# Kernel tuning notes

Measured on AMD Instinct MI355X. Metric: run time of the kernel, lower is better.

The kernel has to match this reference:

```python
import jax
import jax.numpy as jnp
from jax import lax
import numpy as np


def _corr(xs, ks, pad):
    """All-pairs 2D cross-correlation, per sample.

    xs: [N, A, H, W]  (side that gets zero-padded / shifted)
    ks: [N, B, H, W]  (kernels)
    returns out[n, a, b, u, v] = sum_{h,w} xs[n, a, h+u-pad, w+v-pad] * ks[n, b, h, w]
    with u, v in [0, 2*pad].
    """
    xp = jnp.pad(xs, ((0, 0), (0, 0), (pad, pad), (pad, pad)))

    def one(xp1, k1):
        # xp1: [A, H+2p, W+2p] -> lhs batch=A; k1: [B, H, W] -> B output filters
        return lax.conv_general_dilated(
            xp1[:, None], k1[:, None], (1, 1), 'VALID',
            dimension_numbers=('NCHW', 'OIHW', 'NCHW'))  # [A, B, 2p+1-?, ...]

    return jax.vmap(one)(xp, ks)  # [N, A, B, out_h, out_w]


@jax.custom_vjp
def cholesky_solve(Q, P):
    L = jnp.linalg.cholesky(Q)
    return jax.scipy.linalg.cho_solve((L, True), P)


def _chol_fwd(Q, P):
    L = jnp.linalg.cholesky(Q)
    D = jax.scipy.linalg.cho_solve((L, True), P)
    return D, (L, D)


def _chol_bwd(res, g):
    L, D = res
    dP = jax.scipy.linalg.cho_solve((L, True), g)
    dQ = -jnp.matmul(dP, jnp.swapaxes(D, -1, -2))
    return (dQ, dP)


cholesky_solve.defvjp(_chol_fwd, _chol_bwd)


def setup_inputs() -> dict:
    key = jax.random.key(0)
    k1, k2, k3 = jax.random.split(key, 3)
    N, C_in, C_out, H, W, ds = 4, 64, 4, 96, 96, 5
    x = jax.random.normal(k1, (N, 1, C_in, H, W), dtype=jnp.float32)
    d = jax.random.normal(k2, (N, C_out, C_in, ds, ds), dtype=jnp.float32)
    y = jax.random.normal(k3, (N, C_out, 1, H, W), dtype=jnp.float32)
    alpha = jnp.ones((N, 1, 1, 1), dtype=jnp.float32)
    reg = jnp.ones((1,), dtype=jnp.float32)
    return {"x": x, "d": d, "y": y, "alpha": alpha, "reg": reg}


def reference(x, d, y, alpha, reg):
    # DSBlock.forward: solve per-sample regularized normal equations for the dictionary d.
    xs = x[:, 0]      # [N, C_in, H, W]
    ys = y[:, :, 0]   # [N, C_out, H, W]
    N, C_in, H, W = xs.shape
    C_out, ds = d.shape[1], d.shape[-1]
    K = C_in * ds * ds

    # xtx_raw[n, j, i, u, v] = sum_{h,w} x[n,i,h+u-(ds-1), w+v-(ds-1)] * x[n,j,h,w]
    corr = _corr(xs, xs, ds - 1).transpose(0, 2, 1, 3, 4)  # [N, j, i, 2ds-1, 2ds-1]

    # Q[n,(j,kh,kw),(i,ph,pw)] = corr[n,j,i, ph-kh+ds-1, pw-kw+ds-1]
    # (equivalent to the original unfold + flip + fancy-index permutation chain)
    idx = jnp.arange(ds)
    u = idx[None, :] - idx[:, None] + (ds - 1)  # u[k, p] = p - k + ds - 1
    Q6 = corr[:, :, :, u[:, None, :, None], u[None, :, None, :]]  # [N,j,i,kh,kw,ph,pw]
    Q = Q6.transpose(0, 1, 3, 4, 2, 5, 6).reshape(N, K, K)        # symmetric Gram

    # xty[n, i, co, u, v] = sum_{h,w} x[n,i,h+u-p, w+v-p] * y[n,co,h,w], p=(ds-1)//2
    xty = _corr(xs, ys, (ds - 1) // 2)            # [N, i, co, ds, ds]
    P = xty.transpose(0, 1, 3, 4, 2).reshape(N, K, C_out)

    # diagonal regularization: alpha * H * W * reg / (ds^2 * C_in)
    a = alpha.reshape(N) * H * W * reg[0] / (ds * ds * C_in)  # [N]
    Q = Q + a[:, None, None] * jnp.eye(K, dtype=Q.dtype)
    P = P + a[:, None, None] * d.transpose(0, 2, 3, 4, 1).reshape(N, K, C_out)

    D = cholesky_solve(Q, P)                      # [N, K, C_out]
    return D.reshape(N, C_in, ds, ds, C_out).transpose(0, 4, 1, 2, 3)
```

## Files before the change

kernel.cpp:

```cpp
#include <hip/hip_runtime.h>

#define NS   4
#define CIN  64
#define COUT 4
#define HH   96
#define WW   96
#define HWSZ 9216
#define DS   5
#define KD   1600
#define ITER 6

#define TROWB 192
#define TCHB  (96*TROWB)
#define TIMGB ((size_t)64*TCHB)
#define TSB   ((size_t)256*TCHB)
#define CORR_RS 84

#define SKC  12
#define RB   8

#define CSTR  104
#define SLOTB (64*CSTR)

#define XAOFF 0
#define XBOFF 79872
#define XBSLOT (32*CSTR)

typedef _Float16 f16_t;
typedef _Float16 f16x8_t __attribute__((ext_vector_type(8)));
typedef float    f32x16_t __attribute__((ext_vector_type(16)));

static __device__ __forceinline__ float4 f4add(float4 a, float4 b) {
  return make_float4(a.x + b.x, a.y + b.y, a.z + b.z, a.w + b.w);
}
static __device__ __forceinline__ float4 f4sub(float4 a, float4 b) {
  return make_float4(a.x - b.x, a.y - b.y, a.z - b.z, a.w - b.w);
}
static __device__ __forceinline__ float4 f4mul(float4 a, float4 b) {
  return make_float4(a.x * b.x, a.y * b.y, a.z * b.z, a.w * b.w);
}
static __device__ __forceinline__ float4 f4div(float4 a, float4 b) {
  return make_float4(a.x / b.x, a.y / b.y, a.z / b.z, a.w / b.w);
}
static __device__ __forceinline__ float4 f4fma(float4 a, float4 b, float4 c) {
  return make_float4(fmaf(a.x, b.x, c.x), fmaf(a.y, b.y, c.y),
                     fmaf(a.z, b.z, c.z), fmaf(a.w, b.w, c.w));
}
static __device__ __forceinline__ float f4sel(float4 v, int c) {
  return c == 0 ? v.x : c == 1 ? v.y : c == 2 ? v.z : v.w;
}
static __device__ __forceinline__ unsigned int packh2(float a, float b) {
  f16_t h0 = (f16_t)a, h1 = (f16_t)b;
  return (unsigned int)__builtin_bit_cast(unsigned short, h0)
       | ((unsigned int)__builtin_bit_cast(unsigned short, h1) << 16);
}

__global__ __launch_bounds__(256) void convert_kernel(const float* __restrict__ xs,
                                                      const float* __restrict__ ys,
                                                      unsigned int* __restrict__ TS32,
                                                      unsigned int* __restrict__ YS32) {
  const int PER = 256 * 96 * 48;
  const int TSTOT = 5 * PER;
  int idx = blockIdx.x * 256 + threadIdx.x;
  if (idx < TSTOT) {
    int s = idx / PER;
    int rr = idx - s * PER;
    int p = rr % 48; int t = rr / 48;
    int r = t % 96;  int cg = t / 96;
    const float* row = xs + (size_t)cg * HWSZ + r * 96;
    int j0 = 2 * p, j1 = j0 + 1;
    float f0 = (j0 + s < 96) ? row[j0 + s] : 0.f;
    float f1 = (j1 + s < 96) ? row[j1 + s] : 0.f;
    TS32[idx] = packh2(f0, f1);
  } else {
    int i2 = idx - TSTOT;
    if (i2 >= 5 * 16 * 96 * 48) return;
    int v  = i2 / 73728;
    int r3 = i2 % 73728;
    int nb = r3 / 4608;
    int r4 = r3 % 4608;
    int r = r4 / 48, p = r4 % 48;
    const float* row = ys + (size_t)nb * HWSZ + r * 96;
    int c0 = 2 * p + 2 - v, c1 = c0 + 1;
    float f0 = (c0 >= 0 && c0 < 96) ? row[c0] : 0.f;
    float f1 = (c1 >= 0 && c1 < 96) ? row[c1] : 0.f;
    YS32[i2] = packh2(f0, f1);
  }
}

__global__ __launch_bounds__(256, 1) void partial_kernel(const unsigned short* __restrict__ TS,
                                                         const unsigned short* __restrict__ YS,
                                                         float* __restrict__ corrPart,
                                                         float* __restrict__ xtyPart) {
  __shared__ __align__(16) unsigned char lds[24 * SLOTB];
  int bid = blockIdx.x;
  int tid = threadIdx.x, wid = tid >> 6, lane = tid & 63;
  int l5 = lane >> 5, l31 = lane & 31;

  if (bid < 240) {
    int n = bid & 3;
    int rest = bid >> 2;
    int sv = rest % 5;
    int kc = rest / 5;
    int r0 = kc * RB;
    int mt = wid >> 1, nt = wid & 1;
    const char* Abase = (const char*)TS + (size_t)n * TIMGB;
    const char* Bbase = (const char*)TS + (size_t)sv * TSB + (size_t)n * TIMGB;
    f32x16_t acc[9] = {};

    for (int kh = 0; kh < 2; ++kh) {
      if (kh) __syncthreads();
      for (int bb = 0; bb < 3; ++bb) {
        uint4 tmp[12];
#pragma unroll
        for (int i = 0; i < 12; ++i) {
          int q = (bb * 12 + i) * 256 + tid;
          int slot = q / 384;
          int rem = q - slot * 384;
          int ch = rem / 6, sub = rem - ch * 6;
          bool isA = slot < 16;
          int row = isA ? (r0 - 4 + slot) : (r0 + slot - 16);
          uint4 v = make_uint4(0u, 0u, 0u, 0u);
          if (row >= 0 && row < 96) {
            const char* src = (isA ? Abase : Bbase)
                            + (size_t)ch * TCHB + (size_t)row * TROWB + kh * 96 + sub * 16;
            v = *(const uint4*)src;
          }
          tmp[i] = v;
        }
#pragma unroll
        for (int i = 0; i < 12; ++i) {
          int q = (bb * 12 + i) * 256 + tid;
          int slot = q / 384;
          int rem = q - slot * 384;
          int ch = rem / 6, sub = rem - ch * 6;
          char* dst = (char*)lds + slot * SLOTB + ch * CSTR + sub * 16;
          *(uint2*)dst = make_uint2(tmp[i].x, tmp[i].y);
          *(uint2*)(dst + 8) = make_uint2(tmp[i].z, tmp[i].w);
        }
      }
      __syncthreads();

      int ca = mt * 32 + l31, cb = nt * 32 + l31;
#pragma unroll
      for (int ktl = 0; ktl < 3; ++ktl) {
        int ko = ktl * 32 + l5 * 16;
        auto frag = [&](int slot, int ch) -> f16x8_t {
          const char* p = (const char*)lds + slot * SLOTB + ch * CSTR + ko;
          uint2 lo = *(const uint2*)p;
          uint2 hi = *(const uint2*)(p + 8);
          uint4 u = make_uint4(lo.x, lo.y, hi.x, hi.y);
          return __builtin_bit_cast(f16x8_t, u);
        };
        f16x8_t ring[9];
#pragma unroll
        for (int t = 0; t < 9; ++t) ring[t] = frag(t, ca);
#pragma unroll
        for (int r = 0; r < 8; ++r) {
          f16x8_t b = frag(16 + r, cb);
#pragma unroll
          for (int du = 0; du < 9; ++du) {
            acc[du] = __builtin_amdgcn_mfma_f32_32x32x16_f16(
                ring[(r + 8 - du) % 9], b, acc[du], 0, 0, 0);
          }
          if (r < 7) ring[r % 9] = frag(r + 9, ca);
        }
      }
    }
#pragma unroll
    for (int du = 0; du < 9; ++du) {
      float* outp = corrPart + (((size_t)(sv * 9 + du) * SKC + kc) * 4 + n) * 4096;
#pragma unroll
      for (int rg = 0; rg < 16; ++rg) {
        int m  = mt * 32 + (rg & 3) + 8 * (rg >> 2) + 4 * l5;
        int nn = nt * 32 + l31;
        outp[m * 64 + nn] = acc[du][rg];
      }
    }
    return;
  }

  int id = bid - 240;
  int n = id & 3, kc = id >> 2;
  int r0 = kc * RB;
  int mt = wid & 1, rh = wid >> 1;
  const char* Ab = (const char*)TS + (size_t)n * TIMGB;
  const char* Yb = (const char*)YS;
  f32x16_t acc[5] = {};

  for (int kh = 0; kh < 2; ++kh) {
    if (kh) __syncthreads();
    for (int bb = 0; bb < 2; ++bb) {
      uint4 tmp[12];
#pragma unroll
      for (int i = 0; i < 12; ++i) {
        int q = (bb * 12 + i) * 256 + tid;
        uint4 val = make_uint4(0u, 0u, 0u, 0u);
        if (q < 4608) {
          int slot = q / 384, rem = q % 384, ch = rem / 6, sub = rem % 6;
          int grow = r0 - 2 + slot;
          if (grow >= 0 && grow < 96)
            val = *(const uint4*)(Ab + (size_t)ch * TCHB + (size_t)grow * TROWB + kh * 96 + sub * 16);
        } else if (q < 5568) {
          int qq = q - 4608;
          int j = qq / 120, rem = qq % 120, col = rem / 6, sub = rem % 6;
          int b = col / 5, v = col % 5;
          int grow = r0 + j;
          val = *(const uint4*)(Yb + ((size_t)(v * 16 + n * 4 + b) * 96 + grow) * 192 + kh * 96 + sub * 16);
        }
        tmp[i] = val;
      }
#pragma unroll
      for (int i = 0; i < 12; ++i) {
        int q = (bb * 12 + i) * 256 + tid;
        char* dst;
        if (q < 4608) {
          int slot = q / 384, rem = q % 384, ch = rem / 6, sub = rem % 6;
          dst = (char*)lds + XAOFF + slot * SLOTB + ch * CSTR + sub * 16;
        } else {
          int j, col, sub;
          if (q < 5568) { int qq = q - 4608; j = qq / 120; int rem = qq % 120; col = rem / 6; sub = rem % 6; }
          else          { int q2 = q - 5568; j = q2 / 72;  int rem = q2 % 72;  col = 20 + rem / 6; sub = rem % 6; }
          dst = (char*)lds + XBOFF + j * XBSLOT + col * CSTR + sub * 16;
        }
        *(uint2*)dst = make_uint2(tmp[i].x, tmp[i].y);
        *(uint2*)(dst + 8) = make_uint2(tmp[i].z, tmp[i].w);
      }
    }
    __syncthreads();

    int ca = mt * 32 + l31;
    int jb = rh * 4;
#pragma unroll
    for (int ktl = 0; ktl < 3; ++ktl) {
      int ko = ktl * 32 + l5 * 16;
      auto fragA = [&](int slot) -> f16x8_t {
        const char* p = (const char*)lds + XAOFF + slot * SLOTB + ca * CSTR + ko;
        uint2 lo = *(const uint2*)p; uint2 hi = *(const uint2*)(p + 8);
        return __builtin_bit_cast(f16x8_t, make_uint4(lo.x, lo.y, hi.x, hi.y));
      };
      auto fragB = [&](int j) -> f16x8_t {
        const char* p = (const char*)lds + XBOFF + j * XBSLOT + l31 * CSTR + ko;
        uint2 lo = *(const uint2*)p; uint2 hi = *(const uint2*)(p + 8);
        return __builtin_bit_cast(f16x8_t, make_uint4(lo.x, lo.y, hi.x, hi.y));
      };
#pragma unroll
      for (int jj = 0; jj < 4; ++jj) {
        f16x8_t b  = fragB(jb + jj);
        f16x8_t a0 = fragA(jb + jj + 0);
        f16x8_t a1 = fragA(jb + jj + 1);
        f16x8_t a2 = fragA(jb + jj + 2);
        f16x8_t a3 = fragA(jb + jj + 3);
        f16x8_t a4 = fragA(jb + jj + 4);
        acc[0] = __builtin_amdgcn_mfma_f32_32x32x16_f16(a0, b, acc[0], 0, 0, 0);
        acc[1] = __builtin_amdgcn_mfma_f32_32x32x16_f16(a1, b, acc[1], 0, 0, 0);
        acc[2] = __builtin_amdgcn_mfma_f32_32x32x16_f16(a2, b, acc[2], 0, 0, 0);
        acc[3] = __builtin_amdgcn_mfma_f32_32x32x16_f16(a3, b, acc[3], 0, 0, 0);
        acc[4] = __builtin_amdgcn_mfma_f32_32x32x16_f16(a4, b, acc[4], 0, 0, 0);
      }
    }
  }

  __syncthreads();
  float* scr = (float*)lds;
#pragma unroll
  for (int u = 0; u < 5; ++u)
#pragma unroll
    for (int rg = 0; rg < 16; ++rg) {
      int m = mt * 32 + (rg & 3) + 8 * (rg >> 2) + 4 * l5;
      scr[rh * 10240 + u * 2048 + m * 32 + l31] = acc[u][rg];
    }
  __syncthreads();
  float* outp = xtyPart + (size_t)(n * SKC + kc) * 5 * 2048;
  for (int e = tid; e < 10240; e += 256)
    outp[e] = scr[e] + scr[10240 + e];
}

__global__ __launch_bounds__(256) void reduce_kernel(const float* __restrict__ corrPart,
                                                     float* __restrict__ corrP,
                                                     const float* __restrict__ xtyPart,
                                                     const float* __restrict__ dd,
                                                     const float* __restrict__ alpha,
                                                     const float* __restrict__ reg,
                                                     float* __restrict__ P) {
  int bid0 = blockIdx.x;
  if (bid0 < 164) {
    int n = bid0 / 41, p = bid0 % 41;
    int du, dv;
    if (p < 36) { du = p % 9; dv = 5 + p / 9; }
    else        { du = p - 36; dv = 4; }
    int t = (p < 36) ? (9 + p) : (p - 36);
    int o1 = du * 9 + dv, o2 = (8 - du) * 9 + (8 - dv);
    bool mir = !(du == 4 && dv == 4);
    for (int e = threadIdx.x; e < 4096; e += 256) {
      float s = 0.f;
#pragma unroll
      for (int kc = 0; kc < SKC; ++kc)
        s += corrPart[(((size_t)t * SKC + kc) * 4 + n) * 4096 + e];
      int m = e >> 6, nn = e & 63;
      corrP[((size_t)(n * 64 + m) * 64 + nn) * CORR_RS + o1] = s;
      if (mir) corrP[((size_t)(n * 64 + nn) * 64 + m) * CORR_RS + o2] = s;
    }
    return;
  }
  int idx = (bid0 - 164) * 256 + threadIdx.x;
  int b = idx & 3;
  int row = (idx >> 2) % KD;
  int n = idx / 6400;
  int c = row / 25;
  int uv = row % 25;
  int u = uv / 5, v = uv % 5;
  float s = 0.f;
#pragma unroll
  for (int kc = 0; kc < SKC; ++kc)
    s += xtyPart[((size_t)(n * SKC + kc) * 5 + u) * 2048 + c * 32 + b * 5 + v];
  float a = alpha[n] * reg[0] * ((float)(HH * WW) / (float)(DS * DS * CIN));
  float dvv = dd[((size_t)(n * COUT + b) * CIN + c) * 25 + uv];
  P[idx] = s + a * dvv;
}

static __device__ __forceinline__ void allreduce2_f4(float4& a, float4& b,
                                                     float4* redA, float4* redB, int tid) {
#pragma unroll
  for (int off = 1; off < 64; off <<= 1) {
    a.x += __shfl_xor(a.x, off); a.y += __shfl_xor(a.y, off);
    a.z += __shfl_xor(a.z, off); a.w += __shfl_xor(a.w, off);
    b.x += __shfl_xor(b.x, off); b.y += __shfl_xor(b.y, off);
    b.z += __shfl_xor(b.z, off); b.w += __shfl_xor(b.w, off);
  }
  int wid = tid >> 6;
  if ((tid & 63) == 0) { redA[wid] = a; redB[wid] = b; }
  __syncthreads();
  float4 sa = f4add(f4add(redA[0], redA[1]), f4add(redA[2], redA[3]));
  float4 sb = f4add(f4add(redB[0], redB[1]), f4add(redB[2], redB[3]));
  __syncthreads();
  a = sa; b = sb;
}

static __device__ __forceinline__ void allreduce4_f4(float4& a, float4& b, float4& c, float4& d,
                                                     float4 (*red)[4], int tid) {
#pragma unroll
  for (int off = 1; off < 64; off <<= 1) {
    a.x += __shfl_xor(a.x, off); a.y += __shfl_xor(a.y, off);
    a.z += __shfl_xor(a.z, off); a.w += __shfl_xor(a.w, off);
    b.x += __shfl_xor(b.x, off); b.y += __shfl_xor(b.y, off);
    b.z += __shfl_xor(b.z, off); b.w += __shfl_xor(b.w, off);
    c.x += __shfl_xor(c.x, off); c.y += __shfl_xor(c.y, off);
    c.z += __shfl_xor(c.z, off); c.w += __shfl_xor(c.w, off);
    d.x += __shfl_xor(d.x, off); d.y += __shfl_xor(d.y, off);
    d.z += __shfl_xor(d.z, off); d.w += __shfl_xor(d.w, off);
  }
  int wid = tid >> 6;
  if ((tid & 63) == 0) { red[wid][0] = a; red[wid][1] = b; red[wid][2] = c; red[wid][3] = d; }
  __syncthreads();
  float4 sa = f4add(f4add(red[0][0], red[1][0]), f4add(red[2][0], red[3][0]));
  float4 sb = f4add(f4add(red[0][1], red[1][1]), f4add(red[2][1], red[3][1]));
  float4 sc = f4add(f4add(red[0][2], red[1][2]), f4add(red[2][2], red[3][2]));
  float4 sd = f4add(f4add(red[0][3], red[1][3]), f4add(red[2][3], red[3][3]));
  __syncthreads();
  a = sa; b = sb; c = sc; d = sd;
}

__global__ __launch_bounds__(256) void cg_iter_kernel(
    const float* __restrict__ corrP, const float* __restrict__ P,
    const float* __restrict__ Rin, float* __restrict__ Rout,
    const float* __restrict__ Win, float* __restrict__ Wout,
    const float* __restrict__ PFin, float* __restrict__ PFout,
    float* __restrict__ X,
    const float* __restrict__ ralpha, const float* __restrict__ rreg,
    int first) {
  __shared__ float4 pS[KD];
  __shared__ float4 red4[4][4];
  __shared__ float redW[4][25][4];

  int b = blockIdx.x;
  int n = b >> 6, c1 = b & 63;
  int tid = threadIdx.x;

  const float4* Rin4 = (const float4*)Rin + (size_t)n * KD;
  const float4* Win4 = (const float4*)Win + (size_t)n * KD;
  const float4* PFin4 = (const float4*)PFin + (size_t)n * KD;
  const float4* P4 = (const float4*)P + (size_t)n * KD;
  float4* Rout4 = (float4*)Rout + (size_t)n * KD;
  float4* PFout4 = (float4*)PFout + (size_t)n * KD;
  float4* X4 = (float4*)X + (size_t)n * KD;

  const float4 zero4 = make_float4(0.f, 0.f, 0.f, 0.f);
  float4 rv[7], wv[7], pv[7];
#pragma unroll
  for (int t = 0; t < 7; ++t) {
    int idx = tid + 256 * t;
    bool ok = idx < KD;
    if (first) {
      rv[t] = ok ? P4[idx] : zero4;
      wv[t] = zero4; pv[t] = zero4;
    } else {
      rv[t] = ok ? Rin4[idx] : zero4;
      wv[t] = ok ? Win4[idx] : zero4;
      pv[t] = ok ? PFin4[idx] : zero4;
    }
  }
  float4 rho = zero4, pAp = zero4, rw = zero4, ww = zero4;
#pragma unroll
  for (int t = 0; t < 7; ++t) {
    rho = f4fma(rv[t], rv[t], rho);
    pAp = f4fma(pv[t], wv[t], pAp);
    rw  = f4fma(rv[t], wv[t], rw);
    ww  = f4fma(wv[t], wv[t], ww);
  }
  allreduce4_f4(rho, pAp, rw, ww, red4, tid);

  float4 av = first ? zero4 : f4div(rho, pAp);
  float4 two_rw = f4add(rw, rw);
  float4 inner = f4sub(two_rw, f4mul(av, ww));
  float4 rho_k = f4sub(rho, f4mul(av, inner));
  float4 bv = first ? zero4 : f4div(rho_k, rho);

  int lo = c1 * 25;
#pragma unroll
  for (int t = 0; t < 7; ++t) {
    int idx = tid + 256 * t;
    if (idx < KD) {
      rv[t] = f4sub(rv[t], f4mul(av, wv[t]));
      float4 pnew = f4fma(bv, pv[t], rv[t]);
      if (idx >= lo && idx < lo + 25) {
        if (first) X4[idx] = zero4;
        else X4[idx] = f4fma(av, pv[t], X4[idx]);
        PFout4[idx] = pnew;
        Rout4[idx] = rv[t];
      }
      pS[idx] = pnew;
    }
  }
  __syncthreads();

  int c2 = tid >> 2, col = tid & 3;
  const float4* crow4 = (const float4*)(corrP + (((size_t)(n * 64 + c1)) * 64 + c2) * CORR_RS);
  float creg[81];
#pragma unroll
  for (int t4 = 0; t4 < 20; ++t4) *(float4*)&creg[4 * t4] = crow4[t4];
  creg[80] = ((const float*)crow4)[80];

  float a25[25];
#pragma unroll
  for (int i = 0; i < 25; ++i) a25[i] = 0.f;
  const float* pSf = (const float*)pS;
#pragma unroll
  for (int j = 0; j < 25; ++j) {
    float pvv = pSf[(c2 * 25 + j) * 4 + col];
#pragma unroll
    for (int i = 0; i < 25; ++i) {
      const int i1 = i / 5, i2 = i % 5, j1 = j / 5, j2 = j % 5;
      a25[i] += creg[(j1 - i1 + 4) * 9 + (j2 - i2 + 4)] * pvv;
    }
  }
#pragma unroll
  for (int i = 0; i < 25; ++i) {
    float v = a25[i];
    v += __shfl_xor(v, 4); v += __shfl_xor(v, 8);
    v += __shfl_xor(v, 16); v += __shfl_xor(v, 32);
    a25[i] = v;
  }
  int wid = tid >> 6;
  if ((tid & 63) < 4) {
#pragma unroll
    for (int i = 0; i < 25; ++i) redW[wid][i][col] = a25[i];
  }
  __syncthreads();
  if (tid < 100) {
    int i = tid >> 2, cc = tid & 3;
    float wval = redW[0][i][cc] + redW[1][i][cc] + redW[2][i][cc] + redW[3][i][cc];
    float aa = ralpha[n] * rreg[0] * ((float)(HH * WW) / (float)(DS * DS * CIN));
    int row = lo + i;
    wval = fmaf(aa, pSf[row * 4 + cc], wval);
    Wout[((size_t)n * KD + row) * 4 + cc] = wval;
  }
}

__global__ __launch_bounds__(256) void cg_final_kernel(
    const float* __restrict__ Rin, const float* __restrict__ Win,
    const float* __restrict__ PFin, const float* __restrict__ X,
    float* __restrict__ out) {
  __shared__ float4 redA[4], redB[4];
  int b = blockIdx.x;
  int n = b >> 6, c1 = b & 63;
  int tid = threadIdx.x;

  const float4* Rin4 = (const float4*)Rin + (size_t)n * KD;
  const float4* Win4 = (const float4*)Win + (size_t)n * KD;
  const float4* PFin4 = (const float4*)PFin + (size_t)n * KD;
  const float4 zero4 = make_float4(0.f, 0.f, 0.f, 0.f);

  float4 rho = zero4, pAp = zero4;
#pragma unroll
  for (int t = 0; t < 7; ++t) {
    int idx = tid + 256 * t;
    if (idx < KD) {
      float4 r = Rin4[idx], w = Win4[idx], p = PFin4[idx];
      rho = f4fma(r, r, rho);
      pAp = f4fma(p, w, pAp);
    }
  }
  allreduce2_f4(rho, pAp, redA, redB, tid);
  float4 av = f4div(rho, pAp);

  if (tid < 100) {
    int i = tid >> 2, cc = tid & 3;
    int row = c1 * 25 + i;
    float a_cc = f4sel(av, cc);
    float xv = X[((size_t)n * KD + row) * 4 + cc] + a_cc * PFin[((size_t)n * KD + row) * 4 + cc];
    out[((size_t)(n * 4 + cc) * 64 + c1) * 25 + i] = xv;
  }
}

extern "C" void kernel_launch(void* const* d_in, const int* in_sizes, int n_in,
                              void* d_out, int out_size, void* d_ws, size_t ws_size,
                              hipStream_t stream) {
  (void)in_sizes; (void)n_in; (void)out_size; (void)ws_size;
  const float* xs    = (const float*)d_in[0];
  const float* dd    = (const float*)d_in[1];
  const float* ys    = (const float*)d_in[2];
  const float* alpha = (const float*)d_in[3];
  const float* reg   = (const float*)d_in[4];
  float* out = (float*)d_out;
  float* ws  = (float*)d_ws;

  const size_t TS_FLOATS = 5898240;
  const size_t YS_FLOATS = 368640;
  const size_t SZ_CPART = (size_t)45 * SKC * 4 * 4096;
  const size_t SZ_XPART = (size_t)4 * SKC * 5 * 2048;
  const size_t SZ_V = (size_t)NS * KD * COUT;

  unsigned short* TS = (unsigned short*)ws;
  unsigned short* YS = (unsigned short*)(ws + TS_FLOATS);
  float* corrP = ws;
  float* corrPart = ws + TS_FLOATS + YS_FLOATS;
  float* xtyPart = corrPart + SZ_CPART;
  float* P   = xtyPart + SZ_XPART;
  float* X   = P + SZ_V;
  float* R0  = X + SZ_V;
  float* R1  = R0 + SZ_V;
  float* W0  = R1 + SZ_V;
  float* W1  = W0 + SZ_V;
  float* PF0 = W1 + SZ_V;
  float* PF1 = PF0 + SZ_V;
  float* Rb[2] = {R0, R1};
  float* Wb[2] = {W0, W1};
  float* Pb[2] = {PF0, PF1};

  convert_kernel<<<24480, 256, 0, stream>>>(xs, ys, (unsigned int*)TS, (unsigned int*)YS);
  partial_kernel<<<288, 256, 0, stream>>>(TS, YS, corrPart, xtyPart);
  reduce_kernel<<<264, 256, 0, stream>>>(corrPart, corrP, xtyPart, dd, alpha, reg, P);
  for (int k = 0; k < ITER; ++k) {
    cg_iter_kernel<<<NS * CIN, 256, 0, stream>>>(
        corrP, P,
        Rb[k & 1], Rb[(k + 1) & 1],
        Wb[k & 1], Wb[(k + 1) & 1],
        Pb[k & 1], Pb[(k + 1) & 1],
        X, alpha, reg, k == 0 ? 1 : 0);
  }
  cg_final_kernel<<<NS * CIN, 256, 0, stream>>>(Rb[ITER & 1], Wb[ITER & 1], Pb[ITER & 1], X, out);
}
```

Measured before the change: 130.3 us.

## Fuse split-K reduction into partial kernel via last-block atomic counters

Removes the separate reduce kernel. Each partial-kernel block now increments a per-(sample, shift) atomic counter after writing its partial results, and the last of the SKC blocks sums the partials and writes corrP and P. The convert kernel becomes grid-stride with a fixed grid and zeroes the counters. corrP moves to its own workspace region instead of aliasing TS. This saves a launch and overlaps the reduction with the tail of the partial work, but the reduction now runs serially on fewer blocks, and the last-arriving blocks do extra work that may lengthen the tail.

```diff
diff --git a/kernel.cpp b/kernel.cpp
--- a/kernel.cpp
+++ b/kernel.cpp
@@ -55,44 +55,56 @@
        | ((unsigned int)__builtin_bit_cast(unsigned short, h1) << 16);
 }
 
+#define CV_GRID 2048
 __global__ __launch_bounds__(256) void convert_kernel(const float* __restrict__ xs,
                                                       const float* __restrict__ ys,
                                                       unsigned int* __restrict__ TS32,
-                                                      unsigned int* __restrict__ YS32) {
+                                                      unsigned int* __restrict__ YS32,
+                                                      unsigned int* __restrict__ cnt) {
   const int PER = 256 * 96 * 48;
   const int TSTOT = 5 * PER;
-  int idx = blockIdx.x * 256 + threadIdx.x;
-  if (idx < TSTOT) {
-    int s = idx / PER;
-    int rr = idx - s * PER;
-    int p = rr % 48; int t = rr / 48;
-    int r = t % 96;  int cg = t / 96;
-    const float* row = xs + (size_t)cg * HWSZ + r * 96;
-    int j0 = 2 * p, j1 = j0 + 1;
-    float f0 = (j0 + s < 96) ? row[j0 + s] : 0.f;
-    float f1 = (j1 + s < 96) ? row[j1 + s] : 0.f;
-    TS32[idx] = packh2(f0, f1);
-  } else {
-    int i2 = idx - TSTOT;
-    if (i2 >= 5 * 16 * 96 * 48) return;
-    int v  = i2 / 73728;
-    int r3 = i2 % 73728;
-    int nb = r3 / 4608;
-    int r4 = r3 % 4608;
-    int r = r4 / 48, p = r4 % 48;
-    const float* row = ys + (size_t)nb * HWSZ + r * 96;
-    int c0 = 2 * p + 2 - v, c1 = c0 + 1;
-    float f0 = (c0 >= 0 && c0 < 96) ? row[c0] : 0.f;
-    float f1 = (c1 >= 0 && c1 < 96) ? row[c1] : 0.f;
-    YS32[i2] = packh2(f0, f1);
+  const int TOT = TSTOT + 5 * 16 * 96 * 48;
+  int tid0 = blockIdx.x * 256 + threadIdx.x;
+  if (tid0 < 32) cnt[tid0] = 0u;
+  for (int idx = tid0; idx < TOT; idx += CV_GRID * 256) {
+    if (idx < TSTOT) {
+      int s = idx / PER;
+      int rr = idx - s * PER;
+      int p = rr % 48; int t = rr / 48;
+      int r = t % 96;  int cg = t / 96;
+      const float* row = xs + (size_t)cg * HWSZ + r * 96;
+      int j0 = 2 * p, j1 = j0 + 1;
+      float f0 = (j0 + s < 96) ? row[j0 + s] : 0.f;
+      float f1 = (j1 + s < 96) ? row[j1 + s] : 0.f;
+      TS32[idx] = packh2(f0, f1);
+    } else {
+      int i2 = idx - TSTOT;
+      int v  = i2 / 73728;
+      int r3 = i2 % 73728;
+      int nb = r3 / 4608;
+      int r4 = r3 % 4608;
+      int r = r4 / 48, p = r4 % 48;
+      const float* row = ys + (size_t)nb * HWSZ + r * 96;
+      int c0 = 2 * p + 2 - v, c1 = c0 + 1;
+      float f0 = (c0 >= 0 && c0 < 96) ? row[c0] : 0.f;
+      float f1 = (c1 >= 0 && c1 < 96) ? row[c1] : 0.f;
+      YS32[i2] = packh2(f0, f1);
+    }
   }
 }
 
 __global__ __launch_bounds__(256, 1) void partial_kernel(const unsigned short* __restrict__ TS,
                                                          const unsigned short* __restrict__ YS,
                                                          float* __restrict__ corrPart,
-                                                         float* __restrict__ xtyPart) {
+                                                         float* __restrict__ xtyPart,
+                                                         float* __restrict__ corrP,
+                                                         const float* __restrict__ dd,
+                                                         const float* __restrict__ alpha,
+                                                         const float* __restrict__ reg,
+                                                         float* __restrict__ P,
+                                                         unsigned int* __restrict__ cnt) {
   __shared__ __align__(16) unsigned char lds[24 * SLOTB];
+  __shared__ int lastS;
   int bid = blockIdx.x;
   int tid = threadIdx.x, wid = tid >> 6, lane = tid & 63;
   int l5 = lane >> 5, l31 = lane & 31;
@@ -175,6 +187,33 @@
         int m  = mt * 32 + (rg & 3) + 8 * (rg >> 2) + 4 * l5;
         int nn = nt * 32 + l31;
         outp[m * 64 + nn] = acc[du][rg];
+      }
+    }
+
+    __threadfence();
+    __syncthreads();
+    if (tid == 0) {
+      unsigned prev = __hip_atomic_fetch_add(&cnt[n * 5 + sv], 1u,
+                                             __ATOMIC_ACQ_REL, __HIP_MEMORY_SCOPE_AGENT);
+      lastS = (prev == (unsigned)(SKC - 1));
+    }
+    __syncthreads();
+    if (lastS) {
+      int dv = sv + 4;
+      int nDu = (sv == 0) ? 5 : 9;
+      for (int du = 0; du < nDu; ++du) {
+        int t = sv * 9 + du;
+        int o1 = du * 9 + dv, o2 = (8 - du) * 9 + (8 - dv);
+        bool mir = !(du == 4 && dv == 4);
+        for (int e = tid; e < 4096; e += 256) {
+          float s = 0.f;
+#pragma unroll
+          for (int k2 = 0; k2 < SKC; ++k2)
+            s += corrPart[(((size_t)t * SKC + k2) * 4 + n) * 4096 + e];
+          int m = e >> 6, nn = e & 63;
+          corrP[((size_t)(n * 64 + m) * 64 + nn) * CORR_RS + o1] = s;
+          if (mir) corrP[((size_t)(n * 64 + nn) * 64 + m) * CORR_RS + o2] = s;
+        }
       }
     }
     return;
@@ -274,49 +313,31 @@
   float* outp = xtyPart + (size_t)(n * SKC + kc) * 5 * 2048;
   for (int e = tid; e < 10240; e += 256)
     outp[e] = scr[e] + scr[10240 + e];
-}
-
-__global__ __launch_bounds__(256) void reduce_kernel(const float* __restrict__ corrPart,
-                                                     float* __restrict__ corrP,
-                                                     const float* __restrict__ xtyPart,
-                                                     const float* __restrict__ dd,
-                                                     const float* __restrict__ alpha,
-                                                     const float* __restrict__ reg,
-                                                     float* __restrict__ P) {
-  int bid0 = blockIdx.x;
-  if (bid0 < 164) {
-    int n = bid0 / 41, p = bid0 % 41;
-    int du, dv;
-    if (p < 36) { du = p % 9; dv = 5 + p / 9; }
-    else        { du = p - 36; dv = 4; }
-    int t = (p < 36) ? (9 + p) : (p - 36);
-    int o1 = du * 9 + dv, o2 = (8 - du) * 9 + (8 - dv);
-    bool mir = !(du == 4 && dv == 4);
-    for (int e = threadIdx.x; e < 4096; e += 256) {
+
+  __threadfence();
+  __syncthreads();
+  if (tid == 0) {
+    unsigned prev = __hip_atomic_fetch_add(&cnt[20 + n], 1u,
+                                           __ATOMIC_ACQ_REL, __HIP_MEMORY_SCOPE_AGENT);
+    lastS = (prev == (unsigned)(SKC - 1));
+  }
+  __syncthreads();
+  if (lastS) {
+    float a = alpha[n] * reg[0] * ((float)(HH * WW) / (float)(DS * DS * CIN));
+    for (int ii = tid; ii < 6400; ii += 256) {
+      int b = ii & 3;
+      int row = ii >> 2;
+      int c = row / 25;
+      int uv = row % 25;
+      int u = uv / 5, v = uv % 5;
       float s = 0.f;
 #pragma unroll
-      for (int kc = 0; kc < SKC; ++kc)
-        s += corrPart[(((size_t)t * SKC + kc) * 4 + n) * 4096 + e];
-      int m = e >> 6, nn = e & 63;
-      corrP[((size_t)(n * 64 + m) * 64 + nn) * CORR_RS + o1] = s;
-      if (mir) corrP[((size_t)(n * 64 + nn) * 64 + m) * CORR_RS + o2] = s;
-    }
-    return;
-  }
-  int idx = (bid0 - 164) * 256 + threadIdx.x;
-  int b = idx & 3;
-  int row = (idx >> 2) % KD;
-  int n = idx / 6400;
-  int c = row / 25;
-  int uv = row % 25;
-  int u = uv / 5, v = uv % 5;
-  float s = 0.f;
-#pragma unroll
-  for (int kc = 0; kc < SKC; ++kc)
-    s += xtyPart[((size_t)(n * SKC + kc) * 5 + u) * 2048 + c * 32 + b * 5 + v];
-  float a = alpha[n] * reg[0] * ((float)(HH * WW) / (float)(DS * DS * CIN));
-  float dvv = dd[((size_t)(n * COUT + b) * CIN + c) * 25 + uv];
-  P[idx] = s + a * dvv;
+      for (int k2 = 0; k2 < SKC; ++k2)
+        s += xtyPart[((size_t)(n * SKC + k2) * 5 + u) * 2048 + c * 32 + b * 5 + v];
+      float dvv = dd[((size_t)(n * COUT + b) * CIN + c) * 25 + uv];
+      P[((size_t)(n * KD) + row) * 4 + b] = s + a * dvv;
+    }
+  }
 }
 
 static __device__ __forceinline__ void allreduce2_f4(float4& a, float4& b,
@@ -529,14 +550,15 @@
   const size_t YS_FLOATS = 368640;
   const size_t SZ_CPART = (size_t)45 * SKC * 4 * 4096;
   const size_t SZ_XPART = (size_t)4 * SKC * 5 * 2048;
+  const size_t SZ_CORRP = (size_t)NS * 64 * 64 * CORR_RS;
   const size_t SZ_V = (size_t)NS * KD * COUT;
 
   unsigned short* TS = (unsigned short*)ws;
   unsigned short* YS = (unsigned short*)(ws + TS_FLOATS);
-  float* corrP = ws;
   float* corrPart = ws + TS_FLOATS + YS_FLOATS;
   float* xtyPart = corrPart + SZ_CPART;
-  float* P   = xtyPart + SZ_XPART;
+  float* corrP = xtyPart + SZ_XPART;
+  float* P   = corrP + SZ_CORRP;
   float* X   = P + SZ_V;
   float* R0  = X + SZ_V;
   float* R1  = R0 + SZ_V;
@@ -544,13 +566,14 @@
   float* W1  = W0 + SZ_V;
   float* PF0 = W1 + SZ_V;
   float* PF1 = PF0 + SZ_V;
+  unsigned int* cnt = (unsigned int*)(PF1 + SZ_V);
   float* Rb[2] = {R0, R1};
   float* Wb[2] = {W0, W1};
   float* Pb[2] = {PF0, PF1};
 
-  convert_kernel<<<24480, 256, 0, stream>>>(xs, ys, (unsigned int*)TS, (unsigned int*)YS);
-  partial_kernel<<<288, 256, 0, stream>>>(TS, YS, corrPart, xtyPart);
-  reduce_kernel<<<264, 256, 0, stream>>>(corrPart, corrP, xtyPart, dd, alpha, reg, P);
+  convert_kernel<<<CV_GRID, 256, 0, stream>>>(xs, ys, (unsigned int*)TS, (unsigned int*)YS, cnt);
+  partial_kernel<<<288, 256, 0, stream>>>(TS, YS, corrPart, xtyPart,
+                                          corrP, dd, alpha, reg, P, cnt);
   for (int k = 0; k < ITER; ++k) {
     cg_iter_kernel<<<NS * CIN, 256, 0, stream>>>(
         corrP, P,
```

Result: slower. 296.4 us (+127.5%).
